# Optimization experiments

Hardware: AMD Instinct MI355X
Metric: run time of the kernel (lower is better)

## Reference

```python
import jax, jax.numpy as jnp
from jax import lax
import numpy as np

# static config matching init_kwargs
PROPOSAL_COUNT = 1000
NMS_THRESH = 0.7
MIN_SIZE = 16.0
IMG_H, IMG_W = 512, 512
NUM_ANCHORS = 262144
BATCH = 16
PRE_NMS = min(6000, NUM_ANCHORS)


def setup_inputs() -> dict:
    key = jax.random.key(0)
    k1, k2, k3, k4, k5 = jax.random.split(key, 5)
    # realistic anchors: centers uniform in image, sizes in [16, 160]
    cx = jax.random.uniform(k1, (NUM_ANCHORS,), minval=0.0, maxval=float(IMG_W))
    cy = jax.random.uniform(k2, (NUM_ANCHORS,), minval=0.0, maxval=float(IMG_H))
    w = jax.random.uniform(k3, (NUM_ANCHORS,), minval=16.0, maxval=160.0)
    h = jax.random.uniform(k4, (NUM_ANCHORS,), minval=16.0, maxval=160.0)
    anchors = jnp.stack([cx - 0.5 * w, cy - 0.5 * h, cx + 0.5 * w, cy + 0.5 * h], axis=1)
    ka, kb = jax.random.split(k5)
    rpn_class_probs = jax.random.uniform(ka, (BATCH, NUM_ANCHORS, 2), dtype=jnp.float32)
    rpn_bbox_deltas = jax.random.normal(kb, (BATCH, NUM_ANCHORS, 4), dtype=jnp.float32) * 0.2
    return {"anchors": anchors, "rpn_class_probs": rpn_class_probs, "rpn_bbox_deltas": rpn_bbox_deltas}


def apply_box_deltas(anchors, deltas):
    # standard (dx, dy, dw, dh) decode in center form
    w = anchors[:, 2] - anchors[:, 0]
    h = anchors[:, 3] - anchors[:, 1]
    cx = anchors[:, 0] + 0.5 * w
    cy = anchors[:, 1] + 0.5 * h
    cx = cx + deltas[:, 0] * w
    cy = cy + deltas[:, 1] * h
    w = w * jnp.exp(deltas[:, 2])
    h = h * jnp.exp(deltas[:, 3])
    return jnp.stack([cx - 0.5 * w, cy - 0.5 * h, cx + 0.5 * w, cy + 0.5 * h], axis=1)


def nms_keep(boxes, valid):
    # greedy NMS over score-sorted boxes [n,4]; invalid boxes start suppressed
    x1, y1, x2, y2 = boxes[:, 0], boxes[:, 1], boxes[:, 2], boxes[:, 3]
    areas = (x2 - x1) * (y2 - y1)
    n = boxes.shape[0]

    def body(i, state):
        suppressed, keep = state
        is_valid = jnp.logical_not(suppressed[i])
        keep = keep.at[i].set(is_valid)
        xx1 = jnp.maximum(x1[i], x1)
        yy1 = jnp.maximum(y1[i], y1)
        xx2 = jnp.minimum(x2[i], x2)
        yy2 = jnp.minimum(y2[i], y2)
        inter = jnp.maximum(xx2 - xx1, 0.0) * jnp.maximum(yy2 - yy1, 0.0)
        iou = inter / (areas[i] + areas - inter + 1e-9)
        iou = iou.at[i].set(0.0)  # never self-suppress
        suppressed = suppressed | (is_valid & (iou > NMS_THRESH))
        return suppressed, keep

    suppressed0 = jnp.logical_not(valid)
    keep0 = jnp.zeros((n,), dtype=bool)
    _, keep = lax.fori_loop(0, n, body, (suppressed0, keep0))
    return keep


def _per_image(scores, deltas, anchors):
    boxes = apply_box_deltas(anchors, deltas)
    boxes = jnp.stack([
        jnp.clip(boxes[:, 0], 0.0, IMG_W - 1.0),
        jnp.clip(boxes[:, 1], 0.0, IMG_H - 1.0),
        jnp.clip(boxes[:, 2], 0.0, IMG_W - 1.0),
        jnp.clip(boxes[:, 3], 0.0, IMG_H - 1.0),
    ], axis=1)
    ws = boxes[:, 2] - boxes[:, 0]
    hs = boxes[:, 3] - boxes[:, 1]
    valid = (ws >= MIN_SIZE) & (hs >= MIN_SIZE)
    # emulate boolean filter + descending sort with fixed shapes:
    # invalid boxes get -inf score so they sort to the back and start suppressed.
    masked = jnp.where(valid, scores, -jnp.inf)
    order = jnp.argsort(-masked)[:PRE_NMS]
    boxes_s = boxes[order]
    valid_s = valid[order]
    keep = nms_keep(lax.stop_gradient(boxes_s), valid_s)
    idx = jnp.flatnonzero(keep, size=PROPOSAL_COUNT, fill_value=PRE_NMS)
    boxes_pad = jnp.concatenate([boxes_s, jnp.zeros((1, 4), boxes_s.dtype)], axis=0)
    return boxes_pad[idx]  # [proposal_count, 4], zero-padded like torch


def reference(anchors, rpn_class_probs, rpn_bbox_deltas):
    fg_scores = rpn_class_probs[:, :, 1]
    return jax.vmap(_per_image, in_axes=(0, 0, None))(fg_scores, rpn_bbox_deltas, anchors)
```

## Files before the change

### kernel.cpp

```cpp
#include <hip/hip_runtime.h>
#include <cstdint>

#define B 16
#define N 262144
#define PRE 6000
#define KOUT 1000
#define MW 94
#define CW 24
#define NTILE 300
#define ECAP 4096
#define RMAX 64
#define NBIN 2049
#define PREFILT 1967
#define IMGMAX 511.0f
#define NMS_TH 0.7f

typedef unsigned int u32;
typedef unsigned long long u64;

#define OFF_MASK  0ull
#define OFF_SEL   72192000ull
#define OFF_BOX   74289152ull
#define OFF_VAL   75829248ull
#define OFF_HIST  75841536ull
#define OFF_CAB   75972864ull
#define OFF_BCNT  76104192ull
#define OFF_T     76235520ull
#define OFF_M     76235584ull
#define OFF_FLAG  76235648ull
#define OFF_ECNT  76235712ull
#define OFF_EDG   76235776ull
#define OFF_DW    76497920ull
#define OFF_PL    76825600ull
#define OFF_PCNT  78922752ull
#define WS_NEED   78922816ull

__device__ __forceinline__ void box_from(const float4 a, const float4 d,
    float& x1, float& y1, float& x2, float& y2, bool& valid) {
#pragma clang fp contract(off)
  float w  = a.z - a.x;
  float h  = a.w - a.y;
  float cx = a.x + 0.5f * w;
  float cy = a.y + 0.5f * h;
  cx = cx + d.x * w;
  cy = cy + d.y * h;
  w = w * expf(d.z);
  h = h * expf(d.w);
  x1 = cx - 0.5f * w;
  y1 = cy - 0.5f * h;
  x2 = cx + 0.5f * w;
  y2 = cy + 0.5f * h;
  x1 = fminf(fmaxf(x1, 0.0f), IMGMAX);
  y1 = fminf(fmaxf(y1, 0.0f), IMGMAX);
  x2 = fminf(fmaxf(x2, 0.0f), IMGMAX);
  y2 = fminf(fmaxf(y2, 0.0f), IMGMAX);
  valid = ((x2 - x1) >= 16.0f) && ((y2 - y1) >= 16.0f);
}

__device__ __forceinline__ bool iou_gt(float inter, float denom) {
  float d = inter - NMS_TH * denom;
  if (__builtin_expect(fabsf(d) <= 1e-4f * denom, 0))
    return (inter / denom) > NMS_TH;
  return d > 0.0f;
}

__device__ __forceinline__ int bin_of(u32 u) {
  if (u == 0u) return 0;
  float s = __uint_as_float(u & 0x7FFFFFFFu);
  return 1 + min(2047, (int)(s * 2048.0f));
}

__global__ void k_hist(const float4* __restrict__ anch, const float2* __restrict__ probs,
                       const float4* __restrict__ delt, u32* __restrict__ hist,
                       float4* __restrict__ boxes, u64* __restrict__ plist,
                       u32* __restrict__ pcnt) {
  __shared__ u32 sh[NBIN];
  __shared__ u64 pbuf[128];
  __shared__ u32 pcl, pbase;
  int t = threadIdx.x;
  int img = blockIdx.y;
  if (t == 0) pcl = 0;
  if (blockIdx.x == 0 && t < 16)
    boxes[(size_t)img * 6016 + 6000 + t] = make_float4(0.f, 0.f, 0.f, 0.f);
  for (int p = t; p < NBIN; p += 256) sh[p] = 0;
  __syncthreads();
  int base = blockIdx.x * 1024;
  for (int r = 0; r < 4; r++) {
    int i = base + r * 256 + t;
    float4 a = anch[i];
    float4 d = delt[(size_t)img * N + i];
    float s = probs[(size_t)img * N + i].y;
    float x1, y1, x2, y2; bool valid;
    box_from(a, d, x1, y1, x2, y2, valid);
    int bin = valid ? (1 + min(2047, (int)(s * 2048.0f))) : 0;
    atomicAdd(&sh[bin], 1u);
    if (bin >= PREFILT) {
      u64 key = ((u64)(__float_as_uint(s) | 0x80000000u) << 32)
              | (u64)(0xFFFFFFFFu - (u32)i);
      u32 p = atomicAdd(&pcl, 1u);
      if (p < 128u) pbuf[p] = key;
    }
  }
  __syncthreads();
  for (int p = t; p < NBIN; p += 256)
    if (sh[p]) atomicAdd(&hist[img * 2052 + p], sh[p]);
  u32 n = min(pcl, 128u);
  if (t == 0) {
    if (pcl > 128u) atomicAdd(&pcnt[img], 1000000u);
    pbase = n ? atomicAdd(&pcnt[img], n) : 0u;
  }
  __syncthreads();
  for (u32 p = t; p < n; p += 256) {
    u32 dp = pbase + p;
    if (dp < 16384u) plist[(size_t)img * 16384 + dp] = pbuf[p];
  }
}

__global__ void k_thresh(const u32* __restrict__ hist, int* __restrict__ Tarr,
                         u32* __restrict__ cab, u32* __restrict__ Marr) {
  int img = blockIdx.x;
  int l = threadIdx.x;
  const u32* hb = hist + img * 2052;
  u32 v[32];
  u32 csum = 0;
#pragma unroll
  for (int k = 0; k < 32; k++) { v[k] = hb[l * 32 + 1 + k]; csum += v[k]; }
  u32 sfx = csum;
  for (int off = 1; off < 64; off <<= 1) {
    u32 tv = __shfl_down(sfx, off);
    if (l + off < 64) sfx += tv;
  }
  u32 excl = sfx - csum;
  u32 ss = 0;
  u32 outv[32];
#pragma unroll
  for (int k = 31; k >= 0; k--) { outv[k] = ss + excl; ss += v[k]; }
  u32* cb = cab + img * 2052;
#pragma unroll
  for (int k = 0; k < 32; k++) cb[l * 32 + 1 + k] = outv[k];
  u32 total = __shfl(sfx, 0);
  if (l == 0) cb[0] = total;
  if (l == 0 && total < PRE) { Tarr[img] = 0; Marr[img] = 16384u; }
  if (excl < PRE && sfx >= PRE) {
    u32 acc = excl; int T = 0; u32 Mv = 0;
#pragma unroll
    for (int k = 31; k >= 0; k--) {
      acc += v[k];
      if (acc >= PRE) { T = l * 32 + 1 + k; Mv = acc; break; }
    }
    Tarr[img] = T; Marr[img] = Mv;
  }
}

__global__ void k_compact_fast(const u64* __restrict__ plist, const u32* __restrict__ pcnt,
                               const int* __restrict__ Tarr, const u32* __restrict__ cab,
                               u32* __restrict__ bincnt, u64* __restrict__ sel) {
  int t = threadIdx.x, img = blockIdx.y;
  int T = Tarr[img];
  u32 P = pcnt[img];
  if (T < PREFILT || P > 16384u) return;
  const u32* cb = cab + img * 2052;
  for (u32 i = blockIdx.x * 256u + (u32)t; i < P; i += 8u * 256u) {
    u64 key = plist[(size_t)img * 16384 + i];
    int bin = bin_of((u32)(key >> 32));
    if (bin >= T) {
      u32 p = atomicAdd(&bincnt[img * 2052 + bin], 1u);
      u32 dst = cb[bin] + p;
      if (dst < 16384u) sel[(size_t)img * 16384 + dst] = key;
    }
  }
}

__global__ void k_compact_fb(const float4* __restrict__ anch, const float2* __restrict__ probs,
                             const float4* __restrict__ delt, const u32* __restrict__ pcnt,
                             const int* __restrict__ Tarr, const u32* __restrict__ cab,
                             u32* __restrict__ bincnt, u64* __restrict__ sel) {
  int t = threadIdx.x, img = blockIdx.y;
  int T = Tarr[img];
  u32 P = pcnt[img];
  if (T >= PREFILT && P <= 16384u) return;
  const u32* cb = cab + img * 2052;
  for (int chunk = 0; chunk < 32; chunk++) {
    int i = (blockIdx.x * 32 + chunk) * 256 + t;
    float4 a = anch[i];
    float4 d = delt[(size_t)img * N + i];
    float s = probs[(size_t)img * N + i].y;
    float x1, y1, x2, y2; bool valid;
    box_from(a, d, x1, y1, x2, y2, valid);
    int bin = valid ? (1 + min(2047, (int)(s * 2048.0f))) : 0;
    if (bin >= T) {
      u64 key = ((u64)(valid ? (__float_as_uint(s) | 0x80000000u) : 0u) << 32)
              | (u64)(0xFFFFFFFFu - (u32)i);
      u32 p = atomicAdd(&bincnt[img * 2052 + bin], 1u);
      u32 dst = cb[bin] + p;
      if (dst < 16384u) sel[(size_t)img * 16384 + dst] = key;
    }
  }
}

__global__ void k_rank(const u64* __restrict__ sel, const u32* __restrict__ cab,
                       const u32* __restrict__ hist, const u32* __restrict__ Marr,
                       const float4* __restrict__ anch, const float4* __restrict__ delt,
                       float4* __restrict__ boxes, u64* __restrict__ validw) {
  int t = threadIdx.x, img = blockIdx.y;
  u32 M = min(Marr[img], 16384u);
  u32 ci = blockIdx.x * 256u + (u32)t;
  if (ci >= M) return;
  const u64* sb = sel + (size_t)img * 16384;
  u64 key = sb[ci];
  u32 u = (u32)(key >> 32);
  int bin = bin_of(u);
  const u32* cb = cab + img * 2052;
  u32 segs = cb[bin];
  u32 sege;
  if (bin > 0) sege = cb[bin - 1];
  else         sege = min(16384u, segs + hist[img * 2052 + 0]);
  if (sege > 16384u) sege = 16384u;
  u32 within = 0;
  u32 j = segs;
  for (; j + 4 <= sege; j += 4) {
    within += (sb[j]     > key);
    within += (sb[j + 1] > key);
    within += (sb[j + 2] > key);
    within += (sb[j + 3] > key);
  }
  for (; j < sege; j++) within += (sb[j] > key);
  u32 rank = segs + within;
  if (rank < PRE) {
    u32 gi = 0xFFFFFFFFu - (u32)(key & 0xFFFFFFFFull);
    float4 a = anch[gi];
    float4 d = delt[(size_t)img * N + gi];
    float x1, y1, x2, y2; bool valid;
    box_from(a, d, x1, y1, x2, y2, valid);
    boxes[(size_t)img * 6016 + rank] = make_float4(x1, y1, x2, y2);
    if (u != 0u)
      atomicOr(&validw[img * 96 + (rank >> 6)], 1ull << (rank & 63));
  }
}

__global__ void __launch_bounds__(256) k_mask(
    const float4* __restrict__ boxes, u64* __restrict__ dwbuf,
    u32* __restrict__ ecnt, u32* __restrict__ edges) {
  __shared__ float4 cbox[4][64];
  __shared__ float  carea[4][64];
  __shared__ u32 ebuf[4][128];
  __shared__ u32 ecl[4], ebase[4];
  int t = threadIdx.x;
  int l = t & 63, w = t >> 6;
  int img = blockIdx.y;
  int tid = blockIdx.x * 4 + w;
  float disc = (float)((2 * CW + 1) * (2 * CW + 1) - 8 * tid);
  int rb = (int)(((float)(2 * CW + 1) - sqrtf(disc)) * 0.5f);
  if (rb < 0) rb = 0;
  if (rb > CW - 1) rb = CW - 1;
  while (rb > 0 && (rb * CW - (rb * (rb - 1)) / 2) > tid) rb--;
  while (((rb + 1) * CW - ((rb + 1) * rb) / 2) <= tid) rb++;
  int cb = rb + (tid - (rb * CW - (rb * (rb - 1)) / 2));
  if (l == 0) ecl[w] = 0;
  const float4* bb = boxes + (size_t)img * 6016;
  int r = rb * 64 + l;
  float4 rx = bb[r];
  float ra = (rx.z - rx.x) * (rx.w - rx.y);
  float4 c = bb[cb * 64 + l];
  cbox[w][l] = c;
  carea[w][l] = (c.z - c.x) * (c.w - c.y);
  __syncthreads();
  if (cb == rb) {
    u64 bits = 0ull;
    {
#pragma clang fp contract(off)
#pragma unroll 8
      for (int m = 0; m < 64; m++) {
        float4 cx = cbox[w][m];
        float xx1 = fmaxf(rx.x, cx.x);
        float yy1 = fmaxf(rx.y, cx.y);
        float xx2 = fminf(rx.z, cx.z);
        float yy2 = fminf(rx.w, cx.w);
        float inter = fmaxf(xx2 - xx1, 0.0f) * fmaxf(yy2 - yy1, 0.0f);
        float denom = ra + carea[w][m] - inter + 1e-9f;
        if (iou_gt(inter, denom) && m != l) bits |= (1ull << m);
      }
    }
    dwbuf[((size_t)img * CW + cb) * 64 + l] = bits;
  } else {
    {
#pragma clang fp contract(off)
#pragma unroll 8
      for (int m = 0; m < 64; m++) {
        float4 cx = cbox[w][m];
        float xx1 = fmaxf(rx.x, cx.x);
        float yy1 = fmaxf(rx.y, cx.y);
        float xx2 = fminf(rx.z, cx.z);
        float yy2 = fminf(rx.w, cx.w);
        float inter = fmaxf(xx2 - xx1, 0.0f) * fmaxf(yy2 - yy1, 0.0f);
        float denom = ra + carea[w][m] - inter + 1e-9f;
        if (__builtin_expect(iou_gt(inter, denom), 0)) {
          u32 p = atomicAdd(&ecl[w], 1u);
          if (p < 128u) ebuf[w][p] = (((u32)(cb * 64 + m)) << 16) | (u32)r;
        }
      }
    }
    asm volatile("" ::: "memory");
    u32 n = ecl[w];
    if (n == 0u) return;
    if (n > 128u) n = 128u;
    if (l == 0) {
      if (ecl[w] > 128u) atomicAdd(&ecnt[img], 1000000u);
      ebase[w] = atomicAdd(&ecnt[img], n);
    }
    asm volatile("" ::: "memory");
    u32 eb0 = ebase[w];
    for (u32 p = l; p < n; p += 64) {
      u32 dp = eb0 + p;
      if (dp < ECAP) edges[(size_t)img * ECAP + dp] = ebuf[w][p];
    }
  }
}

__global__ void k_mask_rest(const float4* __restrict__ boxes, u64* __restrict__ mask,
                            const u32* __restrict__ okf) {
  int rb = blockIdx.x, img = blockIdx.y;
  if (okf[img]) return;
  __shared__ float4 cbox[4][64];
  __shared__ float  carea[4][64];
  int t = threadIdx.x;
  int rl = t & 63, g = t >> 6;
  const float4* bb = boxes + (size_t)img * 6016;
  int r = rb * 64 + rl;
  float4 rx = bb[r];
  float ra = (rx.z - rx.x) * (rx.w - rx.y);
  u64* mimg = mask + (size_t)img * 94 * 6000;
  int cb0 = rb;
  int jmax = (94 - cb0 + 3) >> 2;
  for (int j = 0; j < jmax; j++) {
    int cb = cb0 + g + 4 * j;
    bool act = cb < 94;
    __syncthreads();
    if (act) {
      float4 c = bb[cb * 64 + rl];
      cbox[g][rl] = c;
      carea[g][rl] = (c.z - c.x) * (c.w - c.y);
    }
    __syncthreads();
    if (act) {
#pragma clang fp contract(off)
      u64 bits = 0ull;
      for (int m = 0; m < 64; m++) {
        float4 cx = cbox[g][m];
        float xx1 = fmaxf(rx.x, cx.x);
        float yy1 = fmaxf(rx.y, cx.y);
        float xx2 = fminf(rx.z, cx.z);
        float yy2 = fminf(rx.w, cx.w);
        float inter = fmaxf(xx2 - xx1, 0.0f) * fmaxf(yy2 - yy1, 0.0f);
        float denom = ra + carea[g][m] - inter + 1e-9f;
        int c_j = cb * 64 + m;
        if (iou_gt(inter, denom) && c_j != r) bits |= (1ull << m);
      }
      if (r < PRE) mimg[(size_t)cb * 6000 + r] = bits;
    }
  }
}

__global__ void __launch_bounds__(64, 1) k_scan_fast(
    const u64* __restrict__ dwbuf, const u64* __restrict__ validw,
    const float4* __restrict__ boxes, float4* __restrict__ out,
    u32* __restrict__ okf, const u32* __restrict__ ecnt,
    const u32* __restrict__ edges) {
  __shared__ u64 dw[CW * 64];
  __shared__ u64 al[CW], fw[CW], kp[CW], blkX[CW], supX[CW];
  __shared__ u32 eb[ECAP];
  __shared__ unsigned short list[KOUT];
  int l = threadIdx.x;
  int img = blockIdx.x;
  for (int c = 0; c < CW; c++)
    dw[c * 64 + l] = dwbuf[((size_t)img * CW + c) * 64 + l];
  u32 E = ecnt[img];
  if (E > (u32)ECAP) { if (l == 0) okf[img] = 0u; return; }
  for (u32 p = l; p < E; p += 64) eb[p] = edges[(size_t)img * ECAP + p];
  if (l < CW) {
    al[l] = validw[img * 96 + l];
    kp[l] = 0ull; blkX[l] = 0ull; supX[l] = 0ull;
  }
  __syncthreads();
  u64 lmask = (1ull << l) - 1ull;
  bool fail = false;
  for (int round = 0; ; round++) {
    u64 anyv = (l < CW) ? al[l] : 0ull;
#pragma unroll
    for (int off = 32; off >= 1; off >>= 1) anyv |= __shfl_xor(anyv, off);
    if (anyv == 0ull) break;
    if (round >= RMAX) { fail = true; break; }
    for (u32 p = l; p < E; p += 64) {
      u32 e = eb[p];
      u32 tgt = e >> 16, src = e & 0xFFFFu;
      if ((al[src >> 6] >> (src & 63u)) & 1ull)
        atomicOr(&blkX[tgt >> 6], 1ull << (tgt & 63u));
    }
    for (int c = 0; c < CW; c++) {
      u64 a_c = al[c];
      u64 dj = dw[c * 64 + l];
      u64 blkin = __ballot((dj & a_c & lmask) != 0ull);
      if (l == 0) fw[c] = a_c & ~blkin & ~blkX[c];
    }
    for (u32 p = l; p < E; p += 64) {
      u32 e = eb[p];
      u32 tgt = e >> 16, src = e & 0xFFFFu;
      if ((fw[src >> 6] >> (src & 63u)) & 1ull)
        atomicOr(&supX[tgt >> 6], 1ull << (tgt & 63u));
    }
    for (int c = 0; c < CW; c++) {
      u64 f_c = fw[c];
      u64 dj = dw[c * 64 + l];
      u64 supin = __ballot((dj & f_c & lmask) != 0ull);
      if (l == 0) {
        kp[c] |= f_c;
        al[c] = al[c] & ~f_c & ~supin & ~supX[c];
      }
    }
    if (l < CW) { blkX[l] = 0ull; supX[l] = 0ull; }
  }
  u64 kw_l = (!fail && l < CW) ? kp[l] : 0ull;
  u32 pc = (u32)__popcll(kw_l);
  u32 pre = pc;
  for (int off = 1; off < 64; off <<= 1) {
    u32 v2 = __shfl_up(pre, off);
    if (l >= off) pre += v2;
  }
  u32 tot = __shfl(pre, 63);
  bool ok = !fail && (tot >= (u32)KOUT);
  if (l == 0) okf[img] = ok ? 1u : 0u;
  if (!ok) return;
  if (l < CW) {
    u32 b = pre - pc;
    u64 word = kw_l;
    while (word && b < (u32)KOUT) {
      int j = (int)__ffsll(word) - 1;
      word &= word - 1;
      list[b++] = (unsigned short)(l * 64 + j);
    }
  }
  __syncthreads();
  for (int p = l; p < KOUT; p += 64)
    out[(size_t)img * KOUT + p] = boxes[(size_t)img * 6016 + list[p]];
}

__global__ void k_scan_full(const u64* __restrict__ mask, const u64* __restrict__ validw,
                            const float4* __restrict__ boxes, float4* __restrict__ out,
                            const u32* __restrict__ okf) {
  int img = blockIdx.x;
  if (okf[img]) return;
  __shared__ unsigned short kept[KOUT];
  int l = threadIdx.x;
  const u64* vw = validw + img * 96;
  u64 r0 = ~vw[l];
  u64 r1 = (l < MW - 64) ? ~vw[64 + l] : ~0ull;
  const u64* c0p = mask + ((size_t)img * 94 + l) * 6000;
  const u64* c1p = mask + ((size_t)img * 94 + (l < MW - 64 ? 64 + l : 0)) * 6000;

  u64 ca[16], cb[16], na[16], nb2[16];
#pragma unroll
  for (int k = 0; k < 16; k++) {
    ca[k] = c0p[k];
    cb[k] = (l < MW - 64) ? c1p[k] : 0ull;
  }
  int cnt = 0; bool done = false;
  for (int base = 0; base < PRE; base += 16) {
#pragma unroll
    for (int k = 0; k < 16; k++) {
      int rr = base + 16 + k;
      if (rr < PRE) {
        na[k]  = c0p[rr];
        nb2[k] = (l < MW - 64) ? c1p[rr] : 0ull;
      } else { na[k] = 0ull; nb2[k] = 0ull; }
    }
#pragma unroll
    for (int k = 0; k < 16; k++) {
      if (!done) {
        int i = base + k;
        int w = i >> 6;
        u64 wv = (w < 64) ? __shfl(r0, w) : __shfl(r1, w - 64);
        if (!((wv >> (i & 63)) & 1ull)) {
          if (l == 0 && cnt < KOUT) kept[cnt] = (unsigned short)i;
          cnt++;
          r0 |= (l >= w)        ? ca[k] : 0ull;
          r1 |= ((64 + l) >= w) ? cb[k] : 0ull;
          if (cnt >= KOUT) done = true;
        }
      }
    }
    if (done) break;
#pragma unroll
    for (int k = 0; k < 16; k++) { ca[k] = na[k]; cb[k] = nb2[k]; }
  }
  __syncthreads();
  for (int p = l; p < KOUT; p += 64) {
    float4 v = make_float4(0.f, 0.f, 0.f, 0.f);
    if (p < cnt) v = boxes[(size_t)img * 6016 + kept[p]];
    out[(size_t)img * KOUT + p] = v;
  }
}

extern "C" void kernel_launch(void* const* d_in, const int* in_sizes, int n_in,
                              void* d_out, int out_size, void* d_ws, size_t ws_size,
                              hipStream_t stream) {
  const float4* anch  = (const float4*)d_in[0];
  const float2* probs = (const float2*)d_in[1];
  const float4* delt  = (const float4*)d_in[2];
  float4* out = (float4*)d_out;
  char* ws = (char*)d_ws;
  (void)in_sizes; (void)n_in;

  if (ws_size < WS_NEED) {
    (void)hipMemsetAsync(d_out, 0, (size_t)out_size * sizeof(float), stream);
    return;
  }

  u64* mask    = (u64*)(ws + OFF_MASK);
  u64* sel     = (u64*)(ws + OFF_SEL);
  float4* bxs  = (float4*)(ws + OFF_BOX);
  u64* validw  = (u64*)(ws + OFF_VAL);
  u32* hist    = (u32*)(ws + OFF_HIST);
  u32* cab     = (u32*)(ws + OFF_CAB);
  u32* bincnt  = (u32*)(ws + OFF_BCNT);
  int* Tarr    = (int*)(ws + OFF_T);
  u32* Marr    = (u32*)(ws + OFF_M);
  u32* okf     = (u32*)(ws + OFF_FLAG);
  u32* ecnt    = (u32*)(ws + OFF_ECNT);
  u32* edges   = (u32*)(ws + OFF_EDG);
  u64* dwbuf   = (u64*)(ws + OFF_DW);
  u64* plist   = (u64*)(ws + OFF_PL);
  u32* pcnt    = (u32*)(ws + OFF_PCNT);

  (void)hipMemsetAsync(ws + OFF_VAL, 0, 406528, stream);
  (void)hipMemsetAsync(ws + OFF_PCNT, 0, 64, stream);

  dim3 g1(256, B);
  k_hist<<<g1, 256, 0, stream>>>(anch, probs, delt, hist, bxs, plist, pcnt);
  k_thresh<<<B, 64, 0, stream>>>(hist, Tarr, cab, Marr);
  dim3 g3(8, B);
  k_compact_fast<<<g3, 256, 0, stream>>>(plist, pcnt, Tarr, cab, bincnt, sel);
  dim3 g3b(32, B);
  k_compact_fb<<<g3b, 256, 0, stream>>>(anch, probs, delt, pcnt, Tarr, cab, bincnt, sel);
  dim3 g4(64, B);
  k_rank<<<g4, 256, 0, stream>>>(sel, cab, hist, Marr, anch, delt, bxs, validw);
  dim3 g5(NTILE / 4, B);
  k_mask<<<g5, 256, 0, stream>>>(bxs, dwbuf, ecnt, edges);
  k_scan_fast<<<B, 64, 0, stream>>>(dwbuf, validw, bxs, out, okf, ecnt, edges);
  dim3 g5b(94, B);
  k_mask_rest<<<g5b, 256, 0, stream>>>(bxs, mask, okf);
  k_scan_full<<<B, 64, 0, stream>>>(mask, validw, bxs, out, okf);
}
```

Measured before the change: 193.9 us.

## Gate histogram pass on score, add fallback full-histogram kernels

The first histogram pass now reads only the score and loads anchors and deltas just for scores at or above a fixed high gate. It histograms only the top 128 bins, and a simplified threshold kernel checks whether those bins already hold the pre-NMS count. If they do not, new fallback kernels rebuild the full histogram and threshold. This is meant to cut the anchor/delta memory traffic and box decoding in the common case, at the cost of two extra kernel launches that exit early.

```diff
diff --git a/kernel.cpp b/kernel.cpp
--- a/kernel.cpp
+++ b/kernel.cpp
@@ -12,6 +12,7 @@
 #define RMAX 64
 #define NBIN 2049
 #define PREFILT 1967
+#define PGATE 0.9599609375f
 #define IMGMAX 511.0f
 #define NMS_TH 0.7f
 
@@ -74,7 +75,7 @@
                        const float4* __restrict__ delt, u32* __restrict__ hist,
                        float4* __restrict__ boxes, u64* __restrict__ plist,
                        u32* __restrict__ pcnt) {
-  __shared__ u32 sh[NBIN];
+  __shared__ u32 sh[128];
   __shared__ u64 pbuf[128];
   __shared__ u32 pcl, pbase;
   int t = threadIdx.x;
@@ -82,6 +83,76 @@
   if (t == 0) pcl = 0;
   if (blockIdx.x == 0 && t < 16)
     boxes[(size_t)img * 6016 + 6000 + t] = make_float4(0.f, 0.f, 0.f, 0.f);
+  if (t < 128) sh[t] = 0;
+  __syncthreads();
+  int base = blockIdx.x * 1024;
+  for (int r = 0; r < 4; r++) {
+    int i = base + r * 256 + t;
+    float s = probs[(size_t)img * N + i].y;
+    if (s >= PGATE) {
+      float4 a = anch[i];
+      float4 d = delt[(size_t)img * N + i];
+      float x1, y1, x2, y2; bool valid;
+      box_from(a, d, x1, y1, x2, y2, valid);
+      if (valid) {
+        int bin = 1 + min(2047, (int)(s * 2048.0f));
+        atomicAdd(&sh[bin - 1921], 1u);
+        u64 key = ((u64)(__float_as_uint(s) | 0x80000000u) << 32)
+                | (u64)(0xFFFFFFFFu - (u32)i);
+        u32 p = atomicAdd(&pcl, 1u);
+        if (p < 128u) pbuf[p] = key;
+      }
+    }
+  }
+  __syncthreads();
+  if (t < 128 && sh[t]) atomicAdd(&hist[img * 2052 + 1921 + t], sh[t]);
+  u32 n = min(pcl, 128u);
+  if (t == 0) {
+    if (pcl > 128u) atomicAdd(&pcnt[img], 1000000u);
+    pbase = n ? atomicAdd(&pcnt[img], n) : 0u;
+  }
+  __syncthreads();
+  for (u32 p = t; p < n; p += 256) {
+    u32 dp = pbase + p;
+    if (dp < 16384u) plist[(size_t)img * 16384 + dp] = pbuf[p];
+  }
+}
+
+__global__ void k_thresh(const u32* __restrict__ hist, int* __restrict__ Tarr,
+                         u32* __restrict__ cab, u32* __restrict__ Marr) {
+  int img = blockIdx.x;
+  int l = threadIdx.x;
+  const u32* hb = hist + img * 2052;
+  u32 v0 = hb[1921 + 2 * l];
+  u32 v1 = hb[1922 + 2 * l];
+  u32 csum = v0 + v1;
+  u32 sfx = csum;
+  for (int off = 1; off < 64; off <<= 1) {
+    u32 tv = __shfl_down(sfx, off);
+    if (l + off < 64) sfx += tv;
+  }
+  u32 excl = sfx - csum;
+  u32* cb = cab + img * 2052;
+  cb[1921 + 2 * l] = excl + v1;
+  cb[1922 + 2 * l] = excl;
+  u32 sfxP = __shfl(excl, 22);
+  bool ok = (sfxP >= (u32)PRE);
+  if (l == 0 && !ok) { Tarr[img] = -1; Marr[img] = 0; }
+  if (ok && excl < (u32)PRE && sfx >= (u32)PRE) {
+    int T; u32 M;
+    if (excl + v1 >= (u32)PRE) { T = 1922 + 2 * l; M = excl + v1; }
+    else                       { T = 1921 + 2 * l; M = sfx; }
+    Tarr[img] = T; Marr[img] = M;
+  }
+}
+
+__global__ void k_hist_fb(const float4* __restrict__ anch, const float2* __restrict__ probs,
+                          const float4* __restrict__ delt, const int* __restrict__ Tarr,
+                          u32* __restrict__ hist) {
+  int img = blockIdx.y;
+  if (Tarr[img] >= 0) return;
+  __shared__ u32 sh[NBIN];
+  int t = threadIdx.x;
   for (int p = t; p < NBIN; p += 256) sh[p] = 0;
   __syncthreads();
   int base = blockIdx.x * 1024;
@@ -93,32 +164,17 @@
     float x1, y1, x2, y2; bool valid;
     box_from(a, d, x1, y1, x2, y2, valid);
     int bin = valid ? (1 + min(2047, (int)(s * 2048.0f))) : 0;
-    atomicAdd(&sh[bin], 1u);
-    if (bin >= PREFILT) {
-      u64 key = ((u64)(__float_as_uint(s) | 0x80000000u) << 32)
-              | (u64)(0xFFFFFFFFu - (u32)i);
-      u32 p = atomicAdd(&pcl, 1u);
-      if (p < 128u) pbuf[p] = key;
-    }
+    if (bin < PREFILT) atomicAdd(&sh[bin], 1u);
   }
   __syncthreads();
   for (int p = t; p < NBIN; p += 256)
     if (sh[p]) atomicAdd(&hist[img * 2052 + p], sh[p]);
-  u32 n = min(pcl, 128u);
-  if (t == 0) {
-    if (pcl > 128u) atomicAdd(&pcnt[img], 1000000u);
-    pbase = n ? atomicAdd(&pcnt[img], n) : 0u;
-  }
-  __syncthreads();
-  for (u32 p = t; p < n; p += 256) {
-    u32 dp = pbase + p;
-    if (dp < 16384u) plist[(size_t)img * 16384 + dp] = pbuf[p];
-  }
-}
-
-__global__ void k_thresh(const u32* __restrict__ hist, int* __restrict__ Tarr,
-                         u32* __restrict__ cab, u32* __restrict__ Marr) {
+}
+
+__global__ void k_thresh_fb(const u32* __restrict__ hist, int* __restrict__ Tarr,
+                            u32* __restrict__ cab, u32* __restrict__ Marr) {
   int img = blockIdx.x;
+  if (Tarr[img] >= 0) return;
   int l = threadIdx.x;
   const u32* hb = hist + img * 2052;
   u32 v[32];
@@ -537,6 +593,8 @@
   dim3 g1(256, B);
   k_hist<<<g1, 256, 0, stream>>>(anch, probs, delt, hist, bxs, plist, pcnt);
   k_thresh<<<B, 64, 0, stream>>>(hist, Tarr, cab, Marr);
+  k_hist_fb<<<g1, 256, 0, stream>>>(anch, probs, delt, Tarr, hist);
+  k_thresh_fb<<<B, 64, 0, stream>>>(hist, Tarr, cab, Marr);
   dim3 g3(8, B);
   k_compact_fast<<<g3, 256, 0, stream>>>(plist, pcnt, Tarr, cab, bincnt, sel);
   dim3 g3b(32, B);
```

Result: faster. 186.3 us (-3.9%).
